# Performance work log

Hardware: AMD Instinct MI355X
Metric: run time of the kernel (lower is better)

Reference implementation:

```python
import jax, jax.numpy as jnp
import numpy as np

B, S, D, H, HD, TOPK = 2, 2048, 2048, 16, 128, 256
HIDDEN = 4 * D
EPS = 1e-6


def setup_inputs() -> dict:
    key = jax.random.key(0)
    ks = jax.random.split(key, 12)
    def g(k, shape, scale):
        return jax.random.normal(k, shape, dtype=jnp.float32) * scale
    # rotary tables: freqs_cis[s, i] = (cos, sin) of s * theta_i
    theta = 1.0 / (10000.0 ** (np.arange(0, HD, 2, dtype=np.float32) / HD))  # [HD/2]
    ang = np.arange(S, dtype=np.float32)[:, None] * theta[None, :]           # [S, HD/2]
    freqs_cis = jnp.asarray(np.stack([np.cos(ang), np.sin(ang)], axis=-1))   # [S, HD/2, 2]
    return {
        "x": g(ks[0], (B, S, D), 1.0),
        "start_pos": 0,
        "freqs_cis": freqs_cis,
        "router_w": g(ks[1], (D, 1), D ** -0.5),
        "wq": g(ks[2], (D, H * HD), D ** -0.5),
        "wk": g(ks[3], (D, H * HD), D ** -0.5),
        "wv": g(ks[4], (D, H * HD), D ** -0.5),
        "wo": g(ks[5], (H * HD, D), (H * HD) ** -0.5),
        "w1": g(ks[6], (D, HIDDEN), D ** -0.5),
        "w2": g(ks[7], (HIDDEN, D), HIDDEN ** -0.5),
        "w3": g(ks[8], (D, HIDDEN), D ** -0.5),
        "attn_norm_w": jnp.ones((D,), jnp.float32),
        "ffn_norm_w": jnp.ones((D,), jnp.float32),
    }


def _rmsnorm(x, w, eps=EPS):
    return x * jax.lax.rsqrt(jnp.mean(x * x, axis=-1, keepdims=True) + eps) * w


def _rotary(q, freqs):  # q: [B,S,H,HD], freqs: [S,HD/2,2]
    q = q.reshape(*q.shape[:-1], HD // 2, 2)
    cos = freqs[None, :, None, :, 0]
    sin = freqs[None, :, None, :, 1]
    qr = q[..., 0] * cos - q[..., 1] * sin
    qi = q[..., 0] * sin + q[..., 1] * cos
    return jnp.stack([qr, qi], axis=-1).reshape(*q.shape[:-2], HD)


def _attention(xn, freqs, tok_mask, wq, wk, wv, wo):
    b, s, _ = xn.shape
    q = (xn @ wq).reshape(b, s, H, HD)
    k = (xn @ wk).reshape(b, s, H, HD)
    v = (xn @ wv).reshape(b, s, H, HD)
    q = _rotary(q, freqs)
    k = _rotary(k, freqs)
    scores = jnp.einsum("bqhd,bkhd->bhqk", q, k) / np.sqrt(HD).astype(np.float32)
    # keys of non-selected tokens are masked out (MoD routing mask)
    scores = scores + jnp.where(tok_mask[:, None, None, :] > 0, 0.0, -1e9)
    attn = jax.nn.softmax(scores, axis=-1)
    out = jnp.einsum("bhqk,bkhd->bqhd", attn, v).reshape(b, s, H * HD)
    return out @ wo


def reference(x, start_pos, freqs_cis, router_w, wq, wk, wv, wo, w1, w2, w3, attn_norm_w, ffn_norm_w):
    b, s, _ = x.shape
    freqs = jax.lax.dynamic_slice_in_dim(freqs_cis, start_pos, s, axis=0)
    # --- router: top-k token selection + scatter mask ---
    token_weights = x @ router_w                      # [B,S,1]
    topk_vals, topk_idx = jax.lax.top_k(token_weights[..., 0], TOPK)
    mask = jnp.zeros((b, s), x.dtype).at[jnp.arange(b)[:, None], topk_idx].set(1.0)
    masked_input = x * mask[:, :, None]
    # --- dense attention + FFN on masked tokens ---
    h = masked_input + _attention(_rmsnorm(masked_input, attn_norm_w), freqs, mask, wq, wk, wv, wo)
    hn = _rmsnorm(h, ffn_norm_w)
    out = (jax.nn.silu(hn @ w1) * (hn @ w3)) @ w2    # SwiGLU FFN
    return out, token_weights, topk_idx
```

## Files before the change

### kernel.cpp

```cpp
#include <hip/hip_runtime.h>
#include <hip/hip_bf16.h>
#include <math.h>

#define B_ 2
#define S_ 2048
#define D_ 2048
#define H_ 16
#define HD_ 128
#define TOPK_ 256
#define HIDDEN_ 8192
#define EPS_ 1e-6f

constexpr int ROWS_SEL = B_ * TOPK_;
constexpr int ROWS_ALL = ROWS_SEL + B_;

typedef __attribute__((ext_vector_type(8))) short bf16x8;
typedef __attribute__((ext_vector_type(4))) float f32x4;

__device__ __forceinline__ short f2bf(float f) {
    __hip_bfloat16 h = __float2bfloat16(f);
    return *reinterpret_cast<short*>(&h);
}

__device__ __forceinline__ float bf2f(short s) {
    union { unsigned u; float f; } c;
    c.u = ((unsigned)(unsigned short)s) << 16;
    return c.f;
}

__device__ __forceinline__ void gll16(const void* g, void* l) {
    __builtin_amdgcn_global_load_lds(
        (const __attribute__((address_space(1))) unsigned int*)g,
        (__attribute__((address_space(3))) unsigned int*)l, 16, 0, 0);
}

__device__ __forceinline__ float block_sum_256(float v, float* red4) {
    for (int o = 32; o; o >>= 1) v += __shfl_down(v, o);
    if ((threadIdx.x & 63) == 0) red4[threadIdx.x >> 6] = v;
    __syncthreads();
    float t = red4[0] + red4[1] + red4[2] + red4[3];
    __syncthreads();
    return t;
}

__device__ __forceinline__ float block_max_256(float v, float* red4) {
    for (int o = 32; o; o >>= 1) v = fmaxf(v, __shfl_down(v, o));
    if ((threadIdx.x & 63) == 0) red4[threadIdx.x >> 6] = v;
    __syncthreads();
    float t = fmaxf(fmaxf(red4[0], red4[1]), fmaxf(red4[2], red4[3]));
    __syncthreads();
    return t;
}

__global__ __launch_bounds__(256) void router_kernel(const float* __restrict__ x,
                                                     const float* __restrict__ rw,
                                                     float* __restrict__ tw) {
    int token = blockIdx.x;
    const float4* xr = (const float4*)(x + (long)token * D_);
    const float4* r4 = (const float4*)rw;
    float s = 0.f;
    for (int c = threadIdx.x; c < D_ / 4; c += 256) {
        float4 a = xr[c], b = r4[c];
        s += a.x * b.x + a.y * b.y + a.z * b.z + a.w * b.w;
    }
    __shared__ float red4[4];
    float tot = block_sum_256(s, red4);
    if (threadIdx.x == 0) tw[token] = tot;
}

__global__ __launch_bounds__(1024) void topk_kernel(const float* __restrict__ tw,
                                                    float* __restrict__ idx_out,
                                                    int* __restrict__ sel_idx,
                                                    int* __restrict__ sel_pos) {
    int b = blockIdx.x;
    __shared__ float v[S_];
    __shared__ int id[S_];
    int t = threadIdx.x;
    for (int i = t; i < S_; i += 1024) {
        v[i] = tw[b * S_ + i];
        id[i] = i;
        sel_pos[b * S_ + i] = -1;
    }
    __syncthreads();
    for (int k = 2; k <= S_; k <<= 1) {
        for (int j = k >> 1; j > 0; j >>= 1) {
            for (int i = t; i < S_; i += 1024) {
                int ixj = i ^ j;
                if (ixj > i) {
                    float va = v[i], vb = v[ixj];
                    int ia = id[i], ib = id[ixj];
                    bool before = (va > vb) || (va == vb && ia < ib);
                    bool dir = ((i & k) == 0);
                    if (dir != before) {
                        v[i] = vb; v[ixj] = va;
                        id[i] = ib; id[ixj] = ia;
                    }
                }
            }
            __syncthreads();
        }
    }
    if (t < TOPK_) {
        idx_out[b * TOPK_ + t] = (float)id[t];
        sel_idx[b * TOPK_ + t] = id[t];
        sel_pos[b * S_ + id[t]] = t;
    }
}

__global__ __launch_bounds__(256) void gather_rmsnorm_kernel(const float* __restrict__ x,
                                                             const int* __restrict__ sel_idx,
                                                             const float* __restrict__ nw,
                                                             short* __restrict__ XN) {
    int r = blockIdx.x;
    int b = r >> 8;
    int s = sel_idx[r];
    const float* xr = x + ((long)b * S_ + s) * D_;
    __shared__ float buf[D_];
    __shared__ float red4[4];
    float ss = 0.f;
    for (int c = threadIdx.x; c < D_; c += 256) {
        float vv = xr[c];
        buf[c] = vv;
        ss += vv * vv;
    }
    float tot = block_sum_256(ss, red4);
    float scale = rsqrtf(tot / D_ + EPS_);
    for (int c = threadIdx.x; c < D_; c += 256)
        XN[(long)r * D_ + c] = f2bf(buf[c] * scale * nw[c]);
}

__global__ __launch_bounds__(256) void gemm_mfma_w(
    const short* __restrict__ A,
    const float* __restrict__ B0, const float* __restrict__ B1, const float* __restrict__ B2,
    float* __restrict__ Cb, long czStride, long spStride,
    int M, int N, int Ktot, int K_per, int splits) {
    __shared__ short As[2][128 * 32];
    __shared__ short Bs[2][128 * 32];
    int z = blockIdx.z;
    int zmat = z / splits, sp = z % splits;
    const float* Bm = (zmat == 0) ? B0 : (zmat == 1) ? B1 : B2;
    float* C = Cb + (long)zmat * czStride + (long)sp * spStride;
    int kbase = sp * K_per;
    int row0 = blockIdx.y * 128, col0 = blockIdx.x * 128;
    int t = threadIdx.x;
    int lane = t & 63, w = t >> 6;
    int l16 = lane & 15, quad = lane >> 4;
    int wr = (w >> 1) * 64, wc = (w & 1) * 64;
    int arr = t >> 2, ach = (t & 3) * 8;
    int bn = t & 127, bkh = (t >> 7) * 16;
    int bswz = (bn >> 1) & 3;
    int bw0o = bn * 32 + ((((bkh >> 3) + 0) ^ bswz) << 3);
    int bw1o = bn * 32 + ((((bkh >> 3) + 1) ^ bswz) << 3);
    const float* bcol = Bm + col0 + bn;
    int ar0 = row0 + arr;      ar0 = (ar0 < M) ? ar0 : (M - 1);
    int ar1 = row0 + arr + 64; ar1 = (ar1 < M) ? ar1 : (M - 1);
    const short* Ap0 = A + (size_t)ar0 * Ktot + ach;
    const short* Ap1 = A + (size_t)ar1 * Ktot + ach;

    f32x4 acc[4][4] = {};
    float f[16];

    {
        const float* src = bcol + (size_t)(kbase + bkh) * N;
        #pragma unroll
        for (int r = 0; r < 16; ++r) f[r] = src[(size_t)r * N];
        gll16(Ap0 + kbase, (char*)As[0] + t * 16);
        gll16(Ap1 + kbase, (char*)As[0] + 4096 + t * 16);
    }

    int nk = K_per >> 5;
    for (int kt = 0; kt < nk; ++kt) {
        int cur = kt & 1;
        short* Bsc = Bs[cur];
        asm volatile("s_waitcnt vmcnt(2)" ::: "memory");
        __builtin_amdgcn_sched_barrier(0);
        union { short s[8]; bf16x8 v; } u0, u1;
        #pragma unroll
        for (int r = 0; r < 8; ++r) u0.s[r] = f2bf(f[r]);
        #pragma unroll
        for (int r = 0; r < 8; ++r) u1.s[r] = f2bf(f[r + 8]);
        *(bf16x8*)(Bsc + bw0o) = u0.v;
        *(bf16x8*)(Bsc + bw1o) = u1.v;
        if (kt + 1 < nk) {
            int k1 = kbase + (kt + 1) * 32;
            const float* src = bcol + (size_t)(k1 + bkh) * N;
            #pragma unroll
            for (int r = 0; r < 16; ++r) f[r] = src[(size_t)r * N];
            char* Adst = (char*)As[cur ^ 1];
            gll16(Ap0 + k1, Adst + t * 16);
            gll16(Ap1 + k1, Adst + 4096 + t * 16);
            asm volatile("s_waitcnt vmcnt(18) lgkmcnt(0)" ::: "memory");
        } else {
            asm volatile("s_waitcnt vmcnt(0) lgkmcnt(0)" ::: "memory");
        }
        __builtin_amdgcn_sched_barrier(0);
        __builtin_amdgcn_s_barrier();
        __builtin_amdgcn_sched_barrier(0);
        const short* Asc = As[cur];
        bf16x8 af[4], bfr[4];
        #pragma unroll
        for (int i = 0; i < 4; ++i)
            af[i] = *(const bf16x8*)(Asc + (wr + i * 16 + l16) * 32 + quad * 8);
        #pragma unroll
        for (int j = 0; j < 4; ++j) {
            int n = wc + j * 16 + l16;
            bfr[j] = *(const bf16x8*)(Bsc + n * 32 + ((quad ^ ((n >> 1) & 3)) << 3));
        }
        #pragma unroll
        for (int i = 0; i < 4; ++i)
            #pragma unroll
            for (int j = 0; j < 4; ++j)
                acc[i][j] = __builtin_amdgcn_mfma_f32_16x16x32_bf16(af[i], bfr[j], acc[i][j], 0, 0, 0);
        __builtin_amdgcn_s_barrier();
        __builtin_amdgcn_sched_barrier(0);
    }
    #pragma unroll
    for (int i = 0; i < 4; ++i) {
        #pragma unroll
        for (int r = 0; r < 4; ++r) {
            int row = row0 + wr + i * 16 + quad * 4 + r;
            if (row < M) {
                #pragma unroll
                for (int j = 0; j < 4; ++j)
                    C[(size_t)row * N + col0 + wc + j * 16 + l16] = acc[i][j][r];
            }
        }
    }
}

template <bool OBF>
__global__ __launch_bounds__(256) void gemm_mfma_attn(
    const short* __restrict__ A, long sAo, long sAi, int lda,
    const short* __restrict__ Bm, long sBo, long sBi, int ldb,
    void* __restrict__ Cv, long sCo, long sCi, int ldc,
    int M, int N, int K, int inner) {
    __shared__ short smem[2 * 128 * 32];
    short* As = smem;
    short* Bs = smem + 128 * 32;
    int z = blockIdx.z;
    int zo = z / inner, zi = z % inner;
    const short* Ab = A + (long)zo * sAo + (long)zi * sAi;
    const short* Bb = Bm + (long)zo * sBo + (long)zi * sBi;
    long cbase = (long)zo * sCo + (long)zi * sCi;
    int row0 = blockIdx.y * 128, col0 = blockIdx.x * 128;
    int t = threadIdx.x;
    int lane = t & 63, w = t >> 6;
    int l16 = lane & 15, quad = lane >> 4;
    int wr = (w >> 1) * 64, wc = (w & 1) * 64;
    int rr = t >> 2, ch = (t & 3) * 8;
    f32x4 acc[4][4] = {};
    for (int k0 = 0; k0 < K; k0 += 32) {
        __syncthreads();
        #pragma unroll
        for (int rd = 0; rd < 2; ++rd) {
            int r = rr + rd * 64;
            int ar = row0 + r; ar = (ar < M) ? ar : (M - 1);
            gll16(Ab + (size_t)ar * lda + k0 + ch, (char*)As + rd * 4096 + t * 16);
            gll16(Bb + (size_t)(col0 + r) * ldb + k0 + ch, (char*)Bs + rd * 4096 + t * 16);
        }
        __syncthreads();
        bf16x8 af[4], bfr[4];
        #pragma unroll
        for (int i = 0; i < 4; ++i)
            af[i] = *(const bf16x8*)(As + (wr + i * 16 + l16) * 32 + quad * 8);
        #pragma unroll
        for (int j = 0; j < 4; ++j)
            bfr[j] = *(const bf16x8*)(Bs + (wc + j * 16 + l16) * 32 + quad * 8);
        #pragma unroll
        for (int i = 0; i < 4; ++i)
            #pragma unroll
            for (int j = 0; j < 4; ++j)
                acc[i][j] = __builtin_amdgcn_mfma_f32_16x16x32_bf16(af[i], bfr[j], acc[i][j], 0, 0, 0);
    }
    #pragma unroll
    for (int i = 0; i < 4; ++i) {
        #pragma unroll
        for (int r = 0; r < 4; ++r) {
            int row = row0 + wr + i * 16 + quad * 4 + r;
            if (row < M) {
                #pragma unroll
                for (int j = 0; j < 4; ++j) {
                    long idx = cbase + (size_t)row * ldc + col0 + wc + j * 16 + l16;
                    if (OBF) ((short*)Cv)[idx] = f2bf(acc[i][j][r]);
                    else     ((float*)Cv)[idx] = acc[i][j][r];
                }
            }
        }
    }
}

__global__ __launch_bounds__(256) void qkv_finish(
    const float* __restrict__ Cp, const float* __restrict__ fc,
    const int* __restrict__ sel_idx, const int* __restrict__ sp0,
    short* __restrict__ Qbf, short* __restrict__ Kbf, short* __restrict__ Vbf,
    int splits) {
    int r = blockIdx.x;
    int s = sel_idx[r];
    int pos = sp0[0] + s;
    const float* f = fc + (long)pos * HD_;
    const long matS = (long)ROWS_SEL * D_;
    const long spS = 3 * matS;
    const float* qp = Cp + (long)r * D_;
    const float* kp = qp + matS;
    const float* vp = qp + 2 * matS;
    const float qscale = 0.08838834764831845f;
    for (int p = threadIdx.x; p < (D_ / 2); p += 256) {
        int h = p >> 6, d2 = p & 63;
        int e0 = h * HD_ + d2 * 2;
        float q0 = 0.f, q1 = 0.f, k0 = 0.f, k1 = 0.f, v0 = 0.f, v1 = 0.f;
        for (int sp = 0; sp < splits; ++sp) {
            long off = (long)sp * spS;
            q0 += qp[off + e0]; q1 += qp[off + e0 + 1];
            k0 += kp[off + e0]; k1 += kp[off + e0 + 1];
            v0 += vp[off + e0]; v1 += vp[off + e0 + 1];
        }
        float c = f[d2 * 2], sn = f[d2 * 2 + 1];
        Qbf[(long)r * D_ + e0]     = f2bf((q0 * c - q1 * sn) * qscale);
        Qbf[(long)r * D_ + e0 + 1] = f2bf((q0 * sn + q1 * c) * qscale);
        Kbf[(long)r * D_ + e0]     = f2bf(k0 * c - k1 * sn);
        Kbf[(long)r * D_ + e0 + 1] = f2bf(k0 * sn + k1 * c);
        Vbf[(long)r * D_ + e0]     = f2bf(v0);
        Vbf[(long)r * D_ + e0 + 1] = f2bf(v1);
    }
}

__global__ __launch_bounds__(256) void vt_kernel(const short* __restrict__ Vbf,
                                                 short* __restrict__ VT) {
    int z = blockIdx.z;
    int b = z >> 4, h = z & 15;
    int key0 = blockIdx.x * 64, d0 = blockIdx.y * 64;
    __shared__ short L[64][72];
    int t = threadIdx.x;
    int kr = t >> 3, dc = (t & 7) * 8;
    #pragma unroll
    for (int rr = 0; rr < 2; ++rr) {
        int key = kr + rr * 32;
        union { short s[8]; int4 v; } u;
        u.v = *(const int4*)&Vbf[(size_t)(b * 256 + key0 + key) * D_ + h * 128 + d0 + dc];
        #pragma unroll
        for (int j = 0; j < 8; ++j) L[key][dc + j] = u.s[j];
    }
    __syncthreads();
    int dr = t >> 3, kc = (t & 7) * 8;
    #pragma unroll
    for (int rr = 0; rr < 2; ++rr) {
        int d = dr + rr * 32;
        union { short s[8]; int4 v; } u;
        #pragma unroll
        for (int j = 0; j < 8; ++j) u.s[j] = L[kc + j][d];
        *(int4*)&VT[((size_t)z * 128 + d0 + d) * 256 + key0 + kc] = u.v;
    }
}

__global__ __launch_bounds__(256) void softmax_kernel(const float* __restrict__ SC,
                                                      short* __restrict__ Pbf) {
    long row = blockIdx.x;
    const float* p = SC + row * 256;
    int t = threadIdx.x;
    float v = p[t];
    __shared__ float red4[4];
    float m = block_max_256(v, red4);
    float e = expf(v - m);
    float s = block_sum_256(e, red4);
    Pbf[row * 256 + t] = f2bf(e / s);
}

__global__ __launch_bounds__(256) void vbar_kernel(const short* __restrict__ Vbf,
                                                   short* __restrict__ Obf) {
    int b = blockIdx.y;
    int c = blockIdx.x * 256 + threadIdx.x;
    float s = 0.f;
    for (int i = 0; i < TOPK_; ++i) s += bf2f(Vbf[((long)b * TOPK_ + i) * D_ + c]);
    Obf[(long)(ROWS_SEL + b) * D_ + c] = f2bf(s * (1.f / TOPK_));
}

__global__ __launch_bounds__(256) void resid_rmsnorm_kernel(const float* __restrict__ Pp,
                                                            int splits,
                                                            const float* __restrict__ x,
                                                            const int* __restrict__ sel_idx,
                                                            const float* __restrict__ nw,
                                                            short* __restrict__ HN) {
    int r = blockIdx.x;
    __shared__ float buf[D_];
    __shared__ float red4[4];
    const long spS = (long)ROWS_ALL * D_;
    const float* pr = Pp + (long)r * D_;
    const float* xr = nullptr;
    if (r < ROWS_SEL) {
        int b = r >> 8;
        int s = sel_idx[r];
        xr = x + ((long)b * S_ + s) * D_;
    }
    float ss = 0.f;
    for (int c = threadIdx.x; c < D_; c += 256) {
        float v = xr ? xr[c] : 0.f;
        for (int sp = 0; sp < splits; ++sp) v += pr[(long)sp * spS + c];
        buf[c] = v;
        ss += v * v;
    }
    float tot = block_sum_256(ss, red4);
    float scale = rsqrtf(tot / D_ + EPS_);
    for (int c = threadIdx.x; c < D_; c += 256)
        HN[(long)r * D_ + c] = f2bf(buf[c] * scale * nw[c]);
}

__global__ __launch_bounds__(256) void reduce_silu_kernel(const float* __restrict__ Gp,
                                                          short* __restrict__ FF, long n) {
    long i = (long)blockIdx.x * 256 + threadIdx.x;
    if (i < n) {
        const long cz = (long)ROWS_ALL * HIDDEN_;
        float a = Gp[i] + Gp[cz + i];
        float g = Gp[2 * cz + i] + Gp[3 * cz + i];
        FF[i] = f2bf((a / (1.f + expf(-a))) * g);
    }
}

__global__ __launch_bounds__(256) void w2_reduce_kernel(const float* __restrict__ Wp,
                                                        float* __restrict__ OUTR, long n4) {
    long i = (long)blockIdx.x * 256 + threadIdx.x;
    if (i < n4) {
        const long spS4 = (long)ROWS_ALL * D_ / 4;
        float4 s = ((const float4*)Wp)[i];
        for (int sp = 1; sp < 8; ++sp) {
            float4 v = ((const float4*)Wp)[(long)sp * spS4 + i];
            s.x += v.x; s.y += v.y; s.z += v.z; s.w += v.w;
        }
        ((float4*)OUTR)[i] = s;
    }
}

__global__ __launch_bounds__(256) void scatter_kernel(const float* __restrict__ OUTR,
                                                      const int* __restrict__ sel_pos,
                                                      float* __restrict__ out) {
    int blk = blockIdx.x;
    int b = blk >> 11;
    int p = sel_pos[blk];
    int row = (p >= 0) ? (b * TOPK_ + p) : (ROWS_SEL + b);
    const float4* src = (const float4*)(OUTR + (long)row * D_);
    float4* dst = (float4*)(out + (long)blk * D_);
    for (int c = threadIdx.x; c < D_ / 4; c += 256) dst[c] = src[c];
}

extern "C" void kernel_launch(void* const* d_in, const int* in_sizes, int n_in,
                              void* d_out, int out_size, void* d_ws, size_t ws_size,
                              hipStream_t stream) {
    const float* x        = (const float*)d_in[0];
    const int*   startpos = (const int*)d_in[1];
    const float* freqs    = (const float*)d_in[2];
    const float* router_w = (const float*)d_in[3];
    const float* wq       = (const float*)d_in[4];
    const float* wk       = (const float*)d_in[5];
    const float* wv       = (const float*)d_in[6];
    const float* wo       = (const float*)d_in[7];
    const float* w1       = (const float*)d_in[8];
    const float* w2       = (const float*)d_in[9];
    const float* w3       = (const float*)d_in[10];
    const float* attn_w   = (const float*)d_in[11];
    const float* ffn_w    = (const float*)d_in[12];

    float* out     = (float*)d_out;
    float* tw_out  = out + (long)B_ * S_ * D_;
    float* idx_out = tw_out + (long)B_ * S_;

    char* ws = (char*)d_ws;
    auto alloc = [&](size_t bytes) -> void* {
        void* p = (void*)ws;
        ws += (bytes + 255) / 256 * 256;
        return p;
    };
    int*   sel_idx = (int*)alloc((size_t)B_ * TOPK_ * sizeof(int));
    int*   sel_pos = (int*)alloc((size_t)B_ * S_ * sizeof(int));
    short* XNbf = (short*)alloc((size_t)ROWS_SEL * D_ * sizeof(short));
    short* Qbf  = (short*)alloc((size_t)ROWS_SEL * D_ * sizeof(short));
    short* Kbf  = (short*)alloc((size_t)ROWS_SEL * D_ * sizeof(short));
    short* Vbf  = (short*)alloc((size_t)ROWS_SEL * D_ * sizeof(short));
    short* VT   = (short*)alloc((size_t)B_ * H_ * HD_ * TOPK_ * sizeof(short));
    float* SC   = (float*)alloc((size_t)B_ * H_ * TOPK_ * TOPK_ * sizeof(float));
    short* Pbf  = (short*)alloc((size_t)B_ * H_ * TOPK_ * TOPK_ * sizeof(short));
    short* Obf  = (short*)alloc((size_t)ROWS_ALL * D_ * sizeof(short));
    short* HNbf = (short*)alloc((size_t)ROWS_ALL * D_ * sizeof(short));
    short* FFbf = (short*)alloc((size_t)ROWS_ALL * HIDDEN_ * sizeof(short));
    float* OUTR = (float*)alloc((size_t)ROWS_ALL * D_ * sizeof(float));
    float* Gar  = (float*)alloc((size_t)4 * ROWS_ALL * HIDDEN_ * sizeof(float));

    router_kernel<<<B_ * S_, 256, 0, stream>>>(x, router_w, tw_out);
    topk_kernel<<<B_, 1024, 0, stream>>>(tw_out, idx_out, sel_idx, sel_pos);
    gather_rmsnorm_kernel<<<ROWS_SEL, 256, 0, stream>>>(x, sel_idx, attn_w, XNbf);
    {
        dim3 g(D_ / 128, ROWS_SEL / 128, 3 * 4);
        gemm_mfma_w<<<g, 256, 0, stream>>>(XNbf, wq, wk, wv,
                                           Gar, (long)ROWS_SEL * D_, (long)3 * ROWS_SEL * D_,
                                           ROWS_SEL, D_, D_, D_ / 4, 4);
    }
    qkv_finish<<<ROWS_SEL, 256, 0, stream>>>(Gar, freqs, sel_idx, startpos, Qbf, Kbf, Vbf, 4);
    {
        dim3 g(4, 2, B_ * H_);
        vt_kernel<<<g, 256, 0, stream>>>(Vbf, VT);
    }
    {
        dim3 g(2, 2, B_ * H_);
        gemm_mfma_attn<false><<<g, 256, 0, stream>>>(
            Qbf, (long)TOPK_ * D_, HD_, D_,
            Kbf, (long)TOPK_ * D_, HD_, D_,
            SC, (long)H_ * TOPK_ * TOPK_, (long)TOPK_ * TOPK_, TOPK_,
            TOPK_, TOPK_, HD_, H_);
    }
    softmax_kernel<<<B_ * H_ * TOPK_, 256, 0, stream>>>(SC, Pbf);
    {
        dim3 g(1, 2, B_ * H_);
        gemm_mfma_attn<true><<<g, 256, 0, stream>>>(
            Pbf, (long)H_ * TOPK_ * TOPK_, (long)TOPK_ * TOPK_, TOPK_,
            VT, (long)H_ * HD_ * TOPK_, (long)HD_ * TOPK_, TOPK_,
            Obf, (long)TOPK_ * D_, HD_, D_,
            TOPK_, HD_, TOPK_, H_);
    }
    {
        dim3 g(D_ / 256, B_, 1);
        vbar_kernel<<<g, 256, 0, stream>>>(Vbf, Obf);
    }
    {
        dim3 g(D_ / 128, (ROWS_ALL + 127) / 128, 8);
        gemm_mfma_w<<<g, 256, 0, stream>>>(Obf, wo, wo, wo,
                                           Gar, 0, (long)ROWS_ALL * D_,
                                           ROWS_ALL, D_, D_, D_ / 8, 8);
    }
    resid_rmsnorm_kernel<<<ROWS_ALL, 256, 0, stream>>>(Gar, 8, x, sel_idx, ffn_w, HNbf);
    {
        dim3 g(HIDDEN_ / 128, (ROWS_ALL + 127) / 128, 2 * 2);
        gemm_mfma_w<<<g, 256, 0, stream>>>(HNbf, w1, w3, w3,
                                           Gar, (long)2 * ROWS_ALL * HIDDEN_, (long)ROWS_ALL * HIDDEN_,
                                           ROWS_ALL, HIDDEN_, D_, D_ / 2, 2);
    }
    {
        long n = (long)ROWS_ALL * HIDDEN_;
        reduce_silu_kernel<<<(unsigned)((n + 255) / 256), 256, 0, stream>>>(Gar, FFbf, n);
    }
    {
        dim3 g(D_ / 128, (ROWS_ALL + 127) / 128, 8);
        gemm_mfma_w<<<g, 256, 0, stream>>>(FFbf, w2, w2, w2,
                                           Gar, 0, (long)ROWS_ALL * D_,
                                           ROWS_ALL, D_, HIDDEN_, HIDDEN_ / 8, 8);
    }
    {
        long n4 = (long)ROWS_ALL * D_ / 4;
        w2_reduce_kernel<<<(unsigned)((n4 + 255) / 256), 256, 0, stream>>>(Gar, OUTR, n4);
    }
    scatter_kernel<<<B_ * S_, 256, 0, stream>>>(OUTR, sel_pos, out);
}
```

Baseline: 559.0 us.

## Deepen fp32 weight prefetch in weight GEMM to two k-tiles ahead

The weight GEMM now keeps two register buffers of fp32 B values and issues global loads two k-steps ahead through inline asm, alternating buffers across an unrolled pair of iterations, with vmcnt waits retuned to match. This aims to hide the latency of the strided fp32 weight loads, which in the old loop were only one tile ahead. It costs 16 extra VGPRs per thread, depends on exact vmcnt counting with hand-written loads, and assumes nk is even.

```diff
diff --git a/kernel.cpp b/kernel.cpp
--- a/kernel.cpp
+++ b/kernel.cpp
@@ -127,6 +127,65 @@
     float scale = rsqrtf(tot / D_ + EPS_);
     for (int c = threadIdx.x; c < D_; c += 256)
         XN[(long)r * D_ + c] = f2bf(buf[c] * scale * nw[c]);
+}
+
+__device__ __forceinline__ void gemm_w_iter(
+    int kt, int nk, int kbase, float (&f)[16],
+    short (*As)[128 * 32], short (*Bs)[128 * 32],
+    int bw0o, int bw1o, const float* bcolk, int N,
+    const short* Ap0, const short* Ap1, int t,
+    int wr, int wc, int l16, int quad, f32x4 (&acc)[4][4]) {
+    int cur = kt & 1;
+    short* Bsc = Bs[cur];
+    if (kt < nk - 1) asm volatile("s_waitcnt vmcnt(18)" ::: "memory");
+    else             asm volatile("s_waitcnt vmcnt(2)" ::: "memory");
+    __builtin_amdgcn_sched_barrier(0);
+    union { short s[8]; bf16x8 v; } u0, u1;
+    #pragma unroll
+    for (int r = 0; r < 8; ++r) u0.s[r] = f2bf(f[r]);
+    #pragma unroll
+    for (int r = 0; r < 8; ++r) u1.s[r] = f2bf(f[r + 8]);
+    *(bf16x8*)(Bsc + bw0o) = u0.v;
+    *(bf16x8*)(Bsc + bw1o) = u1.v;
+    asm volatile("" ::: "memory");
+    if (kt + 1 < nk) {
+        int k1 = kbase + (kt + 1) * 32;
+        char* Adst = (char*)As[(kt + 1) & 1];
+        gll16(Ap0 + k1, Adst + t * 16);
+        gll16(Ap1 + k1, Adst + 4096 + t * 16);
+    }
+    asm volatile("" ::: "memory");
+    if (kt + 2 < nk) {
+        const float* src = bcolk + (size_t)(kbase + (kt + 2) * 32) * N;
+        #pragma unroll
+        for (int r = 0; r < 16; ++r) {
+            const float* a = src + (size_t)r * N;
+            asm volatile("global_load_dword %0, %1, off" : "=v"(f[r]) : "v"(a));
+        }
+    }
+    if (kt < nk - 2)       asm volatile("s_waitcnt vmcnt(34) lgkmcnt(0)" ::: "memory");
+    else if (kt == nk - 2) asm volatile("s_waitcnt vmcnt(18) lgkmcnt(0)" ::: "memory");
+    else                   asm volatile("s_waitcnt vmcnt(0) lgkmcnt(0)" ::: "memory");
+    __builtin_amdgcn_sched_barrier(0);
+    __builtin_amdgcn_s_barrier();
+    __builtin_amdgcn_sched_barrier(0);
+    const short* Asc = As[cur];
+    bf16x8 af[4], bfr[4];
+    #pragma unroll
+    for (int i = 0; i < 4; ++i)
+        af[i] = *(const bf16x8*)(Asc + (wr + i * 16 + l16) * 32 + quad * 8);
+    #pragma unroll
+    for (int j = 0; j < 4; ++j) {
+        int n = wc + j * 16 + l16;
+        bfr[j] = *(const bf16x8*)(Bsc + n * 32 + ((quad ^ ((n >> 1) & 3)) << 3));
+    }
+    #pragma unroll
+    for (int i = 0; i < 4; ++i)
+        #pragma unroll
+        for (int j = 0; j < 4; ++j)
+            acc[i][j] = __builtin_amdgcn_mfma_f32_16x16x32_bf16(af[i], bfr[j], acc[i][j], 0, 0, 0);
+    __builtin_amdgcn_s_barrier();
+    __builtin_amdgcn_sched_barrier(0);
 }
 
 __global__ __launch_bounds__(256) void gemm_mfma_w(
@@ -151,68 +210,40 @@
     int bswz = (bn >> 1) & 3;
     int bw0o = bn * 32 + ((((bkh >> 3) + 0) ^ bswz) << 3);
     int bw1o = bn * 32 + ((((bkh >> 3) + 1) ^ bswz) << 3);
-    const float* bcol = Bm + col0 + bn;
+    const float* bcolk = Bm + col0 + bn + (size_t)bkh * N;
     int ar0 = row0 + arr;      ar0 = (ar0 < M) ? ar0 : (M - 1);
     int ar1 = row0 + arr + 64; ar1 = (ar1 < M) ? ar1 : (M - 1);
     const short* Ap0 = A + (size_t)ar0 * Ktot + ach;
     const short* Ap1 = A + (size_t)ar1 * Ktot + ach;
 
     f32x4 acc[4][4] = {};
-    float f[16];
-
-    {
-        const float* src = bcol + (size_t)(kbase + bkh) * N;
-        #pragma unroll
-        for (int r = 0; r < 16; ++r) f[r] = src[(size_t)r * N];
+    float fA[16], fB[16];
+
+    {
+        const float* src = bcolk + (size_t)kbase * N;
+        #pragma unroll
+        for (int r = 0; r < 16; ++r) {
+            const float* a = src + (size_t)r * N;
+            asm volatile("global_load_dword %0, %1, off" : "=v"(fA[r]) : "v"(a));
+        }
+        asm volatile("" ::: "memory");
         gll16(Ap0 + kbase, (char*)As[0] + t * 16);
         gll16(Ap1 + kbase, (char*)As[0] + 4096 + t * 16);
+        asm volatile("" ::: "memory");
+        const float* src1 = bcolk + (size_t)(kbase + 32) * N;
+        #pragma unroll
+        for (int r = 0; r < 16; ++r) {
+            const float* a = src1 + (size_t)r * N;
+            asm volatile("global_load_dword %0, %1, off" : "=v"(fB[r]) : "v"(a));
+        }
     }
 
     int nk = K_per >> 5;
-    for (int kt = 0; kt < nk; ++kt) {
-        int cur = kt & 1;
-        short* Bsc = Bs[cur];
-        asm volatile("s_waitcnt vmcnt(2)" ::: "memory");
-        __builtin_amdgcn_sched_barrier(0);
-        union { short s[8]; bf16x8 v; } u0, u1;
-        #pragma unroll
-        for (int r = 0; r < 8; ++r) u0.s[r] = f2bf(f[r]);
-        #pragma unroll
-        for (int r = 0; r < 8; ++r) u1.s[r] = f2bf(f[r + 8]);
-        *(bf16x8*)(Bsc + bw0o) = u0.v;
-        *(bf16x8*)(Bsc + bw1o) = u1.v;
-        if (kt + 1 < nk) {
-            int k1 = kbase + (kt + 1) * 32;
-            const float* src = bcol + (size_t)(k1 + bkh) * N;
-            #pragma unroll
-            for (int r = 0; r < 16; ++r) f[r] = src[(size_t)r * N];
-            char* Adst = (char*)As[cur ^ 1];
-            gll16(Ap0 + k1, Adst + t * 16);
-            gll16(Ap1 + k1, Adst + 4096 + t * 16);
-            asm volatile("s_waitcnt vmcnt(18) lgkmcnt(0)" ::: "memory");
-        } else {
-            asm volatile("s_waitcnt vmcnt(0) lgkmcnt(0)" ::: "memory");
-        }
-        __builtin_amdgcn_sched_barrier(0);
-        __builtin_amdgcn_s_barrier();
-        __builtin_amdgcn_sched_barrier(0);
-        const short* Asc = As[cur];
-        bf16x8 af[4], bfr[4];
-        #pragma unroll
-        for (int i = 0; i < 4; ++i)
-            af[i] = *(const bf16x8*)(Asc + (wr + i * 16 + l16) * 32 + quad * 8);
-        #pragma unroll
-        for (int j = 0; j < 4; ++j) {
-            int n = wc + j * 16 + l16;
-            bfr[j] = *(const bf16x8*)(Bsc + n * 32 + ((quad ^ ((n >> 1) & 3)) << 3));
-        }
-        #pragma unroll
-        for (int i = 0; i < 4; ++i)
-            #pragma unroll
-            for (int j = 0; j < 4; ++j)
-                acc[i][j] = __builtin_amdgcn_mfma_f32_16x16x32_bf16(af[i], bfr[j], acc[i][j], 0, 0, 0);
-        __builtin_amdgcn_s_barrier();
-        __builtin_amdgcn_sched_barrier(0);
+    for (int kt = 0; kt < nk; kt += 2) {
+        gemm_w_iter(kt,     nk, kbase, fA, As, Bs, bw0o, bw1o, bcolk, N,
+                    Ap0, Ap1, t, wr, wc, l16, quad, acc);
+        gemm_w_iter(kt + 1, nk, kbase, fB, As, Bs, bw0o, bw1o, bcolk, N,
+                    Ap0, Ap1, t, wr, wc, l16, quad, acc);
     }
     #pragma unroll
     for (int i = 0; i < 4; ++i) {
```

Result: slower. 588.5 us (+5.3%).
